# Performance work log

Measured on AMD Instinct MI355X. Metric: run time of the kernel, lower is better.

## Reference

```python
import jax, jax.numpy as jnp
import numpy as np

NUM_HEADS = 16

def setup_inputs() -> dict:
    key = jax.random.key(0)
    ks = jax.random.split(key, 6)
    B, S, D = 2, 2048, 1024
    x = jax.random.normal(ks[0], (B, S, D), dtype=jnp.float32)
    s = 1.0 / np.sqrt(D)
    Wq = jax.random.normal(ks[1], (D, D), dtype=jnp.float32) * s
    Wk = jax.random.normal(ks[2], (D, D), dtype=jnp.float32) * s
    Wv = jax.random.normal(ks[3], (D, D), dtype=jnp.float32) * s
    Wff = jax.random.normal(ks[4], (D, D), dtype=jnp.float32) * s
    bff = jax.random.normal(ks[5], (D,), dtype=jnp.float32) * 0.01
    return {"x": x, "Wq": Wq, "Wk": Wk, "Wv": Wv, "Wff": Wff, "bff": bff}

def reference(x, Wq, Wk, Wv, Wff, bff):
    B, S, D = x.shape
    H = NUM_HEADS
    Dh = D // H
    # Q/K/V projections (bias-free Linears). Original scales Q by 1/sqrt(hidden_size).
    q = (x @ Wq.T) * (1.0 / jnp.sqrt(jnp.asarray(D, x.dtype)))
    k = x @ Wk.T
    v = x @ Wv.T
    q = q.reshape(B, S, H, Dh)
    k = k.reshape(B, S, H, Dh)
    v = v.reshape(B, S, H, Dh)
    # Blockwise online-softmax attention is mathematically identical to
    # full softmax attention over all keys (no causal mask in source).
    scores = jnp.einsum('bqhd,bkhd->bhqk', q, k)
    attn = jax.nn.softmax(scores, axis=-1)
    out = jnp.einsum('bhqk,bkhd->bqhd', attn, v).reshape(B, S, D)
    # Final feedforward Linear(hidden, hidden) with bias.
    return out @ Wff.T + bff
```

## Files before the change

### kernel.cpp

```cpp
#include <hip/hip_runtime.h>
#include <stdint.h>

typedef __attribute__((ext_vector_type(8))) short bf16x8;
typedef __attribute__((ext_vector_type(4))) float f32x4;

__device__ __forceinline__ uint16_t f2bf(float f) {
  union { float f; uint32_t u; } a; a.f = f;
  uint32_t u = a.u;
  u += 0x7FFFu + ((u >> 16) & 1u);
  return (uint16_t)(u >> 16);
}

__device__ __forceinline__ uint32_t pk_bf16(float a, float b) {
#if __has_builtin(__builtin_amdgcn_cvt_pk_bf16_f32)
  auto r = __builtin_amdgcn_cvt_pk_bf16_f32(a, b);
  uint32_t u; __builtin_memcpy(&u, &r, sizeof(u));
  return u;
#else
  return (uint32_t)f2bf(a) | ((uint32_t)f2bf(b) << 16);
#endif
}

__device__ __forceinline__ uint32_t pk_bf16_fast(float a, float b) {
#if __has_builtin(__builtin_amdgcn_cvt_pk_bf16_f32)
  auto r = __builtin_amdgcn_cvt_pk_bf16_f32(a, b);
  uint32_t u; __builtin_memcpy(&u, &r, sizeof(u));
  return u;
#else
  uint32_t ua, ub;
  __builtin_memcpy(&ua, &a, 4); __builtin_memcpy(&ub, &b, 4);
  return __builtin_amdgcn_perm(ub, ua, 0x07060302u);
#endif
}

__device__ __forceinline__ float fast_exp2(float x) {
#if __has_builtin(__builtin_amdgcn_exp2f)
  return __builtin_amdgcn_exp2f(x);
#else
  return exp2f(x);
#endif
}

__device__ __forceinline__ void gld_lds16(const uint16_t* g, uint16_t* l) {
  __builtin_amdgcn_global_load_lds(
      (const __attribute__((address_space(1))) void*)g,
      (__attribute__((address_space(3))) void*)l, 16, 0, 0);
}

__global__ void cast_all(const float* __restrict__ x, const float* __restrict__ wq,
                         const float* __restrict__ wk, const float* __restrict__ wv,
                         const float* __restrict__ wff,
                         uint16_t* __restrict__ xb, uint16_t* __restrict__ wqb,
                         uint16_t* __restrict__ wkb, uint16_t* __restrict__ wvb,
                         uint16_t* __restrict__ wffb) {
  int i = blockIdx.x * blockDim.x + threadIdx.x;
  const float* src; uint16_t* dst; int off;
  if (i < 1048576)      { src = x;   dst = xb;   off = i; }
  else if (i < 1310720) { src = wq;  dst = wqb;  off = i - 1048576; }
  else if (i < 1572864) { src = wk;  dst = wkb;  off = i - 1310720; }
  else if (i < 1835008) { src = wv;  dst = wvb;  off = i - 1572864; }
  else                  { src = wff; dst = wffb; off = i - 1835008; }
  float4 v = ((const float4*)src)[off];
  uint2 o; o.x = pk_bf16(v.x, v.y); o.y = pk_bf16(v.z, v.w);
  ((uint2*)dst)[off] = o;
}

__device__ __forceinline__ void gemm_tile(const uint16_t* __restrict__ Abase,
                                          const uint16_t* __restrict__ Bbase,
                                          uint16_t* lds, f32x4 acc[4][4]) {
  const int tid  = threadIdx.x;
  const int w    = tid >> 6;
  const int lane = tid & 63;
  const int wm   = w >> 1, wn = w & 1;
  const int lrow = lane & 15;
  const int quad = lane >> 4;
  const int srow = lane >> 3;
  const int lc   = (lane & 7) ^ srow;
  const int sx   = lrow & 7;
  uint16_t* a_lds = lds;
  uint16_t* b_lds = lds + 8192;

#pragma unroll
  for (int mt = 0; mt < 4; ++mt)
#pragma unroll
    for (int nt = 0; nt < 4; ++nt)
      acc[mt][nt] = (f32x4){0.f, 0.f, 0.f, 0.f};

  const uint16_t* ag = Abase + (size_t)(w * 32 + srow) * 1024 + lc * 8;
  const uint16_t* bg = Bbase + (size_t)(w * 32 + srow) * 1024 + lc * 8;

  for (int k0 = 0; k0 < 1024; k0 += 64) {
#pragma unroll
    for (int i8 = 0; i8 < 4; ++i8) {
      gld_lds16(ag + (size_t)i8 * 8 * 1024 + k0, a_lds + (w * 4 + i8) * 512);
      gld_lds16(bg + (size_t)i8 * 8 * 1024 + k0, b_lds + (w * 4 + i8) * 512);
    }
    __syncthreads();
#pragma unroll
    for (int ks = 0; ks < 2; ++ks) {
      bf16x8 af[4], bfr[4];
      const int c = ((ks * 4 + quad) ^ sx) << 3;
#pragma unroll
      for (int mt = 0; mt < 4; ++mt)
        af[mt] = *(const bf16x8*)(a_lds + (wm * 64 + mt * 16 + lrow) * 64 + c);
#pragma unroll
      for (int nt = 0; nt < 4; ++nt)
        bfr[nt] = *(const bf16x8*)(b_lds + (wn * 64 + nt * 16 + lrow) * 64 + c);
#pragma unroll
      for (int mt = 0; mt < 4; ++mt)
#pragma unroll
        for (int nt = 0; nt < 4; ++nt)
          acc[mt][nt] = __builtin_amdgcn_mfma_f32_16x16x32_bf16(af[mt], bfr[nt], acc[mt][nt], 0, 0, 0);
    }
    __syncthreads();
  }
}

__global__ __launch_bounds__(256) void gemm_qkv(
    const uint16_t* __restrict__ x,
    const uint16_t* __restrict__ wq, const uint16_t* __restrict__ wk, const uint16_t* __restrict__ wv,
    uint16_t* __restrict__ qo, uint16_t* __restrict__ ko, uint16_t* __restrict__ vto) {
  __shared__ __align__(16) uint16_t lds[17408];
  const int m0 = blockIdx.x * 128, n0 = blockIdx.y * 128, z = blockIdx.z;
  f32x4 acc[4][4];
  if (z < 2) {
    const uint16_t* W = (z == 0) ? wq : wk;
    gemm_tile(W + (size_t)n0 * 1024, x + (size_t)m0 * 1024, lds, acc);
  } else {
    gemm_tile(x + (size_t)m0 * 1024, wv + (size_t)n0 * 1024, lds, acc);
  }

  const int tid = threadIdx.x;
  const int lane = tid & 63, w = tid >> 6;
  const int wm = w >> 1, wn = w & 1, lrow = lane & 15, quad = lane >> 4;
  const float scale = (z == 0) ? 0.045084222f : 1.0f;

#pragma unroll
  for (int mt = 0; mt < 4; ++mt)
#pragma unroll
    for (int nt = 0; nt < 4; ++nt) {
      int i0 = wm * 64 + mt * 16 + quad * 4;
      int j  = wn * 64 + nt * 16 + lrow;
      uint2 dd;
      dd.x = pk_bf16(acc[mt][nt][0] * scale, acc[mt][nt][1] * scale);
      dd.y = pk_bf16(acc[mt][nt][2] * scale, acc[mt][nt][3] * scale);
      *(uint2*)(&lds[j * 136 + i0]) = dd;
    }
  __syncthreads();

  uint16_t* outp = (z == 0) ? qo : (z == 1) ? ko : vto;
  if (z < 2) {
#pragma unroll
    for (int it = 0; it < 8; ++it) {
      int idx = it * 256 + tid;
      int jj = idx >> 4, cc = idx & 15;
      uint4 v = *(const uint4*)(&lds[jj * 136 + cc * 8]);
      int m = m0 + jj, n = n0 + cc * 8;
      int b = m >> 11, s = m & 2047, h = n >> 6, dh = n & 63;
      *(uint4*)(outp + ((size_t)((b * 16 + h) * 2048 + s)) * 64 + dh) = v;
    }
  } else {
    int b = m0 >> 11, sbase = m0 & 2047;
#pragma unroll
    for (int it = 0; it < 8; ++it) {
      int idx = it * 256 + tid;
      int ff = idx >> 4, cc = idx & 15;
      uint4 v = *(const uint4*)(&lds[ff * 136 + cc * 8]);
      int n = n0 + ff, h = n >> 6, dh = n & 63;
      *(uint4*)(outp + ((size_t)((b * 16 + h) * 64 + dh)) * 2048 + sbase + cc * 8) = v;
    }
  }
}

__global__ __launch_bounds__(256) void gemm_ff(
    const uint16_t* __restrict__ ao, const uint16_t* __restrict__ wff,
    const float* __restrict__ bff, float* __restrict__ out) {
  __shared__ __align__(16) uint16_t lds[17408];
  const int m0 = blockIdx.x * 128, n0 = blockIdx.y * 128;
  f32x4 acc[4][4];
  gemm_tile(wff + (size_t)n0 * 1024, ao + (size_t)m0 * 1024, lds, acc);

  const int tid = threadIdx.x;
  const int lane = tid & 63, w = tid >> 6;
  const int wm = w >> 1, wn = w & 1, lrow = lane & 15, quad = lane >> 4;
  float* fl = (float*)lds;

#pragma unroll
  for (int p = 0; p < 2; ++p) {
    if (wm == p) {
#pragma unroll
      for (int mt = 0; mt < 4; ++mt)
#pragma unroll
        for (int nt = 0; nt < 4; ++nt) {
          int i0 = mt * 16 + quad * 4;
          int j  = wn * 64 + nt * 16 + lrow;
          *(f32x4*)(&fl[j * 68 + i0]) = acc[mt][nt];
        }
    }
    __syncthreads();
#pragma unroll
    for (int it = 0; it < 8; ++it) {
      int idx = it * 256 + tid;
      int jj = idx >> 4, cc = idx & 15;
      f32x4 v = *(const f32x4*)(&fl[jj * 68 + cc * 4]);
      int n = n0 + p * 64 + cc * 4;
      f32x4 bias = *(const f32x4*)(bff + n);
      f32x4 vv = v + bias;
      *(f32x4*)(out + (size_t)(m0 + jj) * 1024 + n) = vv;
    }
    __syncthreads();
  }
}

__global__ __launch_bounds__(128, 2) void attn(
    const uint16_t* __restrict__ q, const uint16_t* __restrict__ k,
    const uint16_t* __restrict__ vt, uint16_t* __restrict__ ao) {
  __shared__ __align__(16) uint16_t k_lds[2][4096];
  __shared__ __align__(16) uint16_t v_lds[2][4096];
  __shared__ __align__(16) uint16_t p_lds[2][4096];
  const int tid = threadIdx.x, w = tid >> 6, lane = tid & 63;
  const int lrow = lane & 15, quad = lane >> 4;
  const int srow = lane >> 3, lc = (lane & 7) ^ srow, sx = lrow & 7;
  const int bh = blockIdx.y, qb = blockIdx.x;
  const uint16_t* Q = q  + (size_t)bh * (2048 * 64);
  const uint16_t* K = k  + (size_t)bh * (2048 * 64);
  const uint16_t* V = vt + (size_t)bh * (64 * 2048);
  uint16_t* pw = p_lds[w];
  const int cswz = (lrow & 7) << 1;

  const int qr0 = qb * 128 + w * 64;
  bf16x8 qf[4][2];
#pragma unroll
  for (int qh = 0; qh < 4; ++qh)
#pragma unroll
    for (int ks = 0; ks < 2; ++ks)
      qf[qh][ks] = *(const bf16x8*)(Q + (size_t)(qr0 + qh * 16 + lrow) * 64 + ks * 32 + quad * 8);

  f32x4 o[4][4];
#pragma unroll
  for (int qh = 0; qh < 4; ++qh)
#pragma unroll
    for (int dt = 0; dt < 4; ++dt) o[qh][dt] = (f32x4){0.f, 0.f, 0.f, 0.f};
  float ls[4] = {0.f, 0.f, 0.f, 0.f};

  auto stage = [&](int kb, int bi) {
#pragma unroll
    for (int i4 = 0; i4 < 4; ++i4) {
      int i8 = w * 4 + i4;
      gld_lds16(K + (size_t)(kb * 64 + i8 * 8 + srow) * 64 + lc * 8, &k_lds[bi][i8 * 512]);
      gld_lds16(V + (size_t)(i8 * 8 + srow) * 2048 + kb * 64 + lc * 8, &v_lds[bi][i8 * 512]);
    }
  };
  stage(0, 0);

  for (int kb = 0; kb < 32; ++kb) {
    const int bi = kb & 1;
    __syncthreads();
    if (kb + 1 < 32) stage(kb + 1, bi ^ 1);

    f32x4 s[4][4];
#pragma unroll
    for (int qh = 0; qh < 4; ++qh)
#pragma unroll
      for (int kt = 0; kt < 4; ++kt) s[qh][kt] = (f32x4){0.f, 0.f, 0.f, 0.f};
#pragma unroll
    for (int ks = 0; ks < 2; ++ks) {
      const int c = ((ks * 4 + quad) ^ sx) << 3;
#pragma unroll
      for (int kt = 0; kt < 4; ++kt) {
        bf16x8 kf = *(const bf16x8*)(&k_lds[bi][(kt * 16 + lrow) * 64 + c]);
#pragma unroll
        for (int qh = 0; qh < 4; ++qh)
          s[qh][kt] = __builtin_amdgcn_mfma_f32_16x16x32_bf16(kf, qf[qh][ks], s[qh][kt], 0, 0, 0);
      }
    }

#pragma unroll
    for (int qh = 0; qh < 4; ++qh)
#pragma unroll
      for (int kt = 0; kt < 4; ++kt) {
        float p0 = fast_exp2(s[qh][kt][0]);
        float p1 = fast_exp2(s[qh][kt][1]);
        float p2 = fast_exp2(s[qh][kt][2]);
        float p3 = fast_exp2(s[qh][kt][3]);
        ls[qh] += (p0 + p1) + (p2 + p3);
        uint2 dd; dd.x = pk_bf16_fast(p0, p1); dd.y = pk_bf16_fast(p2, p3);
        *(uint2*)(pw + (qh * 16 + lrow) * 64 + (((kt * 4 + quad) ^ cswz) << 2)) = dd;
      }

#pragma unroll
    for (int ks = 0; ks < 2; ++ks) {
      bf16x8 pa[4];
#pragma unroll
      for (int qh = 0; qh < 4; ++qh)
        pa[qh] = *(const bf16x8*)(pw + (qh * 16 + lrow) * 64 + (((ks * 8 + quad * 2) ^ cswz) << 2));
      const int c = ((ks * 4 + quad) ^ sx) << 3;
#pragma unroll
      for (int dt = 0; dt < 4; ++dt) {
        bf16x8 vf = *(const bf16x8*)(&v_lds[bi][(dt * 16 + lrow) * 64 + c]);
#pragma unroll
        for (int qh = 0; qh < 4; ++qh)
          o[qh][dt] = __builtin_amdgcn_mfma_f32_16x16x32_bf16(vf, pa[qh], o[qh][dt], 0, 0, 0);
      }
    }
  }

  const int b = bh >> 4, h = bh & 15;
#pragma unroll
  for (int qh = 0; qh < 4; ++qh) {
    float l = ls[qh];
    l += __shfl_xor(l, 16);
    l += __shfl_xor(l, 32);
    float inv = 1.0f / l;
    int sg = qr0 + qh * 16 + lrow;
#pragma unroll
    for (int dt = 0; dt < 4; ++dt) {
      uint2 dd;
      dd.x = pk_bf16(o[qh][dt][0] * inv, o[qh][dt][1] * inv);
      dd.y = pk_bf16(o[qh][dt][2] * inv, o[qh][dt][3] * inv);
      *(uint2*)(ao + (size_t)(b * 2048 + sg) * 1024 + h * 64 + dt * 16 + quad * 4) = dd;
    }
  }
}

extern "C" void kernel_launch(void* const* d_in, const int* in_sizes, int n_in,
                              void* d_out, int out_size, void* d_ws, size_t ws_size,
                              hipStream_t stream) {
  const float* x   = (const float*)d_in[0];
  const float* Wq  = (const float*)d_in[1];
  const float* Wk  = (const float*)d_in[2];
  const float* Wv  = (const float*)d_in[3];
  const float* Wff = (const float*)d_in[4];
  const float* bff = (const float*)d_in[5];
  float* out = (float*)d_out;

  uint16_t* ws = (uint16_t*)d_ws;
  uint16_t* x_bf   = ws;
  uint16_t* wq_bf  = ws + 4194304;
  uint16_t* wk_bf  = ws + 5242880;
  uint16_t* wv_bf  = ws + 6291456;
  uint16_t* wff_bf = ws + 7340032;
  uint16_t* q_bf   = ws + 8388608;
  uint16_t* k_bf   = ws + 12582912;
  uint16_t* vt_bf  = ws + 16777216;
  uint16_t* ao_bf  = ws + 20971520;

  cast_all<<<8192, 256, 0, stream>>>(x, Wq, Wk, Wv, Wff, x_bf, wq_bf, wk_bf, wv_bf, wff_bf);

  gemm_qkv<<<dim3(32, 8, 3), 256, 0, stream>>>(x_bf, wq_bf, wk_bf, wv_bf, q_bf, k_bf, vt_bf);
  attn<<<dim3(16, 32), 128, 0, stream>>>(q_bf, k_bf, vt_bf, ao_bf);
  gemm_ff<<<dim3(32, 8), 256, 0, stream>>>(ao_bf, wff_bf, bff, out);
}
```

Before: 210.0 us.

## Split attention work across four waves with shared P tile and deferred PV

The attention kernel moves from 2 to 4 waves per block. For QK^T each wave now takes a 16-key slice for all 128 queries. For PV each wave takes a (query half, key half) pair, reading a shared block-wide P tile from double-buffered LDS. The PV product is deferred by one iteration so that it overlaps the next block's load. Partial O sums and row sums are then reduced through LDS at the end. This buys more waves in flight, at the cost of more LDS, extra P traffic, and a final cross-wave reduction.

```diff
diff --git a/kernel.cpp b/kernel.cpp
--- a/kernel.cpp
+++ b/kernel.cpp
@@ -212,26 +212,26 @@
   }
 }
 
-__global__ __launch_bounds__(128, 2) void attn(
+__global__ __launch_bounds__(256, 2) void attn(
     const uint16_t* __restrict__ q, const uint16_t* __restrict__ k,
     const uint16_t* __restrict__ vt, uint16_t* __restrict__ ao) {
   __shared__ __align__(16) uint16_t k_lds[2][4096];
   __shared__ __align__(16) uint16_t v_lds[2][4096];
-  __shared__ __align__(16) uint16_t p_lds[2][4096];
+  __shared__ __align__(16) uint16_t p_lds[2][8192];
   const int tid = threadIdx.x, w = tid >> 6, lane = tid & 63;
   const int lrow = lane & 15, quad = lane >> 4;
   const int srow = lane >> 3, lc = (lane & 7) ^ srow, sx = lrow & 7;
+  const int pk = w >> 1, pq = w & 1;
+  const int pswz = (lrow & 3) << 2;
   const int bh = blockIdx.y, qb = blockIdx.x;
   const uint16_t* Q = q  + (size_t)bh * (2048 * 64);
   const uint16_t* K = k  + (size_t)bh * (2048 * 64);
   const uint16_t* V = vt + (size_t)bh * (64 * 2048);
-  uint16_t* pw = p_lds[w];
-  const int cswz = (lrow & 7) << 1;
-
-  const int qr0 = qb * 128 + w * 64;
-  bf16x8 qf[4][2];
-#pragma unroll
-  for (int qh = 0; qh < 4; ++qh)
+
+  const int qr0 = qb * 128;
+  bf16x8 qf[8][2];
+#pragma unroll
+  for (int qh = 0; qh < 8; ++qh)
 #pragma unroll
     for (int ks = 0; ks < 2; ++ks)
       qf[qh][ks] = *(const bf16x8*)(Q + (size_t)(qr0 + qh * 16 + lrow) * 64 + ks * 32 + quad * 8);
@@ -241,12 +241,13 @@
   for (int qh = 0; qh < 4; ++qh)
 #pragma unroll
     for (int dt = 0; dt < 4; ++dt) o[qh][dt] = (f32x4){0.f, 0.f, 0.f, 0.f};
-  float ls[4] = {0.f, 0.f, 0.f, 0.f};
+  float ls[8] = {0.f, 0.f, 0.f, 0.f, 0.f, 0.f, 0.f, 0.f};
+  bf16x8 vfr[4];
 
   auto stage = [&](int kb, int bi) {
 #pragma unroll
-    for (int i4 = 0; i4 < 4; ++i4) {
-      int i8 = w * 4 + i4;
+    for (int i2 = 0; i2 < 2; ++i2) {
+      int i8 = w * 2 + i2;
       gld_lds16(K + (size_t)(kb * 64 + i8 * 8 + srow) * 64 + lc * 8, &k_lds[bi][i8 * 512]);
       gld_lds16(V + (size_t)(i8 * 8 + srow) * 2048 + kb * 64 + lc * 8, &v_lds[bi][i8 * 512]);
     }
@@ -256,69 +257,100 @@
   for (int kb = 0; kb < 32; ++kb) {
     const int bi = kb & 1;
     __syncthreads();
+
+    if (kb > 0) {
+      const uint16_t* pbuf = p_lds[bi ^ 1];
+#pragma unroll
+      for (int qh = 0; qh < 4; ++qh) {
+        int row = pq * 64 + qh * 16 + lrow;
+        bf16x8 pa = *(const bf16x8*)(pbuf + row * 64 + (((pk * 8 + quad * 2) ^ pswz) << 2));
+#pragma unroll
+        for (int dt = 0; dt < 4; ++dt)
+          o[qh][dt] = __builtin_amdgcn_mfma_f32_16x16x32_bf16(vfr[dt], pa, o[qh][dt], 0, 0, 0);
+      }
+    }
+
+#pragma unroll
+    for (int dt = 0; dt < 4; ++dt)
+      vfr[dt] = *(const bf16x8*)(&v_lds[bi][(dt * 16 + lrow) * 64 + (((pk * 4 + quad) ^ sx) << 3)]);
+
     if (kb + 1 < 32) stage(kb + 1, bi ^ 1);
 
-    f32x4 s[4][4];
+    f32x4 s[8];
+#pragma unroll
+    for (int qh = 0; qh < 8; ++qh) s[qh] = (f32x4){0.f, 0.f, 0.f, 0.f};
+#pragma unroll
+    for (int ks = 0; ks < 2; ++ks) {
+      bf16x8 kf = *(const bf16x8*)(&k_lds[bi][(w * 16 + lrow) * 64 + (((ks * 4 + quad) ^ sx) << 3)]);
+#pragma unroll
+      for (int qh = 0; qh < 8; ++qh)
+        s[qh] = __builtin_amdgcn_mfma_f32_16x16x32_bf16(kf, qf[qh][ks], s[qh], 0, 0, 0);
+    }
+
+    uint16_t* pbw = p_lds[bi];
+#pragma unroll
+    for (int qh = 0; qh < 8; ++qh) {
+      float p0 = fast_exp2(s[qh][0]);
+      float p1 = fast_exp2(s[qh][1]);
+      float p2 = fast_exp2(s[qh][2]);
+      float p3 = fast_exp2(s[qh][3]);
+      ls[qh] += (p0 + p1) + (p2 + p3);
+      uint2 dd; dd.x = pk_bf16_fast(p0, p1); dd.y = pk_bf16_fast(p2, p3);
+      int row = qh * 16 + lrow;
+      *(uint2*)(pbw + row * 64 + (((w * 4 + quad) ^ pswz) << 2)) = dd;
+    }
+  }
+
+  __syncthreads();
+  {
+    const uint16_t* pbuf = p_lds[1];
+#pragma unroll
+    for (int qh = 0; qh < 4; ++qh) {
+      int row = pq * 64 + qh * 16 + lrow;
+      bf16x8 pa = *(const bf16x8*)(pbuf + row * 64 + (((pk * 8 + quad * 2) ^ pswz) << 2));
+#pragma unroll
+      for (int dt = 0; dt < 4; ++dt)
+        o[qh][dt] = __builtin_amdgcn_mfma_f32_16x16x32_bf16(vfr[dt], pa, o[qh][dt], 0, 0, 0);
+    }
+  }
+  __syncthreads();
+
+#pragma unroll
+  for (int qh = 0; qh < 8; ++qh) {
+    ls[qh] += __shfl_xor(ls[qh], 16);
+    ls[qh] += __shfl_xor(ls[qh], 32);
+  }
+  float* lred  = (float*)&k_lds[0][0];
+  float* arena = (float*)&p_lds[0][0];
+  if (quad == 0) {
+#pragma unroll
+    for (int qh = 0; qh < 8; ++qh) lred[w * 128 + qh * 16 + lrow] = ls[qh];
+  }
+  if (pk == 1) {
 #pragma unroll
     for (int qh = 0; qh < 4; ++qh)
 #pragma unroll
-      for (int kt = 0; kt < 4; ++kt) s[qh][kt] = (f32x4){0.f, 0.f, 0.f, 0.f};
-#pragma unroll
-    for (int ks = 0; ks < 2; ++ks) {
-      const int c = ((ks * 4 + quad) ^ sx) << 3;
-#pragma unroll
-      for (int kt = 0; kt < 4; ++kt) {
-        bf16x8 kf = *(const bf16x8*)(&k_lds[bi][(kt * 16 + lrow) * 64 + c]);
-#pragma unroll
-        for (int qh = 0; qh < 4; ++qh)
-          s[qh][kt] = __builtin_amdgcn_mfma_f32_16x16x32_bf16(kf, qf[qh][ks], s[qh][kt], 0, 0, 0);
+      for (int dt = 0; dt < 4; ++dt)
+        *(f32x4*)(&arena[(pq * 64 + qh * 16 + lrow) * 64 + dt * 16 + quad * 4]) = o[qh][dt];
+  }
+  __syncthreads();
+
+  if (pk == 0) {
+    const int b = bh >> 4, h = bh & 15;
+#pragma unroll
+    for (int qh = 0; qh < 4; ++qh) {
+      int qrow = pq * 64 + qh * 16 + lrow;
+      float l = lred[qrow] + lred[128 + qrow] + lred[256 + qrow] + lred[384 + qrow];
+      float inv = 1.0f / l;
+      int sg = qr0 + qrow;
+#pragma unroll
+      for (int dt = 0; dt < 4; ++dt) {
+        f32x4 a = *(const f32x4*)(&arena[qrow * 64 + dt * 16 + quad * 4]);
+        uint2 dd;
+        dd.x = pk_bf16((o[qh][dt][0] + a[0]) * inv, (o[qh][dt][1] + a[1]) * inv);
+        dd.y = pk_bf16((o[qh][dt][2] + a[2]) * inv, (o[qh][dt][3] + a[3]) * inv);
+        *(uint2*)(ao + (size_t)(b * 2048 + sg) * 1024 + h * 64 + dt * 16 + quad * 4) = dd;
       }
-    }
-
-#pragma unroll
-    for (int qh = 0; qh < 4; ++qh)
-#pragma unroll
-      for (int kt = 0; kt < 4; ++kt) {
-        float p0 = fast_exp2(s[qh][kt][0]);
-        float p1 = fast_exp2(s[qh][kt][1]);
-        float p2 = fast_exp2(s[qh][kt][2]);
-        float p3 = fast_exp2(s[qh][kt][3]);
-        ls[qh] += (p0 + p1) + (p2 + p3);
-        uint2 dd; dd.x = pk_bf16_fast(p0, p1); dd.y = pk_bf16_fast(p2, p3);
-        *(uint2*)(pw + (qh * 16 + lrow) * 64 + (((kt * 4 + quad) ^ cswz) << 2)) = dd;
-      }
-
-#pragma unroll
-    for (int ks = 0; ks < 2; ++ks) {
-      bf16x8 pa[4];
-#pragma unroll
-      for (int qh = 0; qh < 4; ++qh)
-        pa[qh] = *(const bf16x8*)(pw + (qh * 16 + lrow) * 64 + (((ks * 8 + quad * 2) ^ cswz) << 2));
-      const int c = ((ks * 4 + quad) ^ sx) << 3;
-#pragma unroll
-      for (int dt = 0; dt < 4; ++dt) {
-        bf16x8 vf = *(const bf16x8*)(&v_lds[bi][(dt * 16 + lrow) * 64 + c]);
-#pragma unroll
-        for (int qh = 0; qh < 4; ++qh)
-          o[qh][dt] = __builtin_amdgcn_mfma_f32_16x16x32_bf16(vf, pa[qh], o[qh][dt], 0, 0, 0);
-      }
-    }
-  }
-
-  const int b = bh >> 4, h = bh & 15;
-#pragma unroll
-  for (int qh = 0; qh < 4; ++qh) {
-    float l = ls[qh];
-    l += __shfl_xor(l, 16);
-    l += __shfl_xor(l, 32);
-    float inv = 1.0f / l;
-    int sg = qr0 + qh * 16 + lrow;
-#pragma unroll
-    for (int dt = 0; dt < 4; ++dt) {
-      uint2 dd;
-      dd.x = pk_bf16(o[qh][dt][0] * inv, o[qh][dt][1] * inv);
-      dd.y = pk_bf16(o[qh][dt][2] * inv, o[qh][dt][3] * inv);
-      *(uint2*)(ao + (size_t)(b * 2048 + sg) * 1024 + h * 64 + dt * 16 + quad * 4) = dd;
     }
   }
 }
@@ -348,6 +380,6 @@
   cast_all<<<8192, 256, 0, stream>>>(x, Wq, Wk, Wv, Wff, x_bf, wq_bf, wk_bf, wv_bf, wff_bf);
 
   gemm_qkv<<<dim3(32, 8, 3), 256, 0, stream>>>(x_bf, wq_bf, wk_bf, wv_bf, q_bf, k_bf, vt_bf);
-  attn<<<dim3(16, 32), 128, 0, stream>>>(q_bf, k_bf, vt_bf, ao_bf);
+  attn<<<dim3(16, 32), 256, 0, stream>>>(q_bf, k_bf, vt_bf, ao_bf);
   gemm_ff<<<dim3(32, 8), 256, 0, stream>>>(ao_bf, wff_bf, bff, out);
 }
```

Result: faster. 183.4 us (-12.7%).
